# Optimization experiments

Measured on AMD Instinct MI355X. Metric: run time of the kernel, lower is better.

## Reference

```python
import jax, jax.numpy as jnp
import numpy as np
from jax import lax

NUM_SKETCH = 3
BN_EPS = 1e-5


def setup_inputs() -> dict:
    key = jax.random.key(0)
    ks = jax.random.split(key, 8)
    B, C, H, W = 32, 128, 64, 64
    D = C // 4  # comp_rate = 4
    k = 3
    x = jax.random.normal(ks[0], (B, C, H, W), dtype=jnp.float32)
    fan = C * k * k
    w1 = jax.random.normal(ks[1], (C, C, k, k), dtype=jnp.float32) / np.sqrt(fan)
    w2 = jax.random.normal(ks[2], (C, C, k, k), dtype=jnp.float32) / np.sqrt(fan)
    gamma1 = jnp.ones((C,), jnp.float32); beta1 = jnp.zeros((C,), jnp.float32)
    gamma2 = jnp.ones((C,), jnp.float32); beta2 = jnp.zeros((C,), jnp.float32)
    # count-sketch hash matrices: hs[j] is (D, C), each column c has a single 1
    idx = jax.random.randint(ks[3], (NUM_SKETCH, C), 0, D)
    hs = jax.nn.one_hot(idx, D, dtype=jnp.float32).transpose(0, 2, 1)  # (3, D, C)
    ss = (jax.random.randint(ks[4], (NUM_SKETCH, C), 0, 2) * 2 - 1).astype(jnp.float32)  # (3, C) signs
    return {"x": x, "w1": w1, "w2": w2, "gamma1": gamma1, "beta1": beta1,
            "gamma2": gamma2, "beta2": beta2, "hs": hs, "ss": ss}


def _sketch_conv_unsketch(x, w, hs, ss):
    # w: (Co, Ci, k, k); hs: (J, D, Co); ss: (J, Co)
    Co, Ci, k, _ = w.shape
    J, D, _ = hs.shape
    B, _, H, W = x.shape
    wf = w.reshape(Co, -1)  # (Co, M)
    # sketched weights per sketch j: h_j @ (wf * s_j[:, None])
    w_sk = jnp.einsum('jdc,jc,cm->jdm', hs, ss, wf).reshape(J * D, Ci, k, k)
    # one conv with J*D output channels (padding=1, stride=1 hardcoded in source)
    y = lax.conv_general_dilated(x, w_sk, window_strides=(1, 1),
                                 padding=[(1, 1), (1, 1)],
                                 dimension_numbers=('NCHW', 'OIHW', 'NCHW'))
    y = y.reshape(B, J, D, H, W)
    # unsketch activations: h_j^T @ y_j, then sign scale (num_s=1 so inner median is identity)
    y_un = jnp.einsum('jdc,bjdhw->jbchw', hs, y) * ss[:, None, :, None, None]
    return jnp.median(y_un, axis=0)  # median over the 3 sketches -> (B, Co, H, W)


def _bn_relu(y, gamma, beta):
    # BatchNorm2d in training mode: biased batch stats over (N, H, W)
    mean = jnp.mean(y, axis=(0, 2, 3), keepdims=True)
    var = jnp.var(y, axis=(0, 2, 3), keepdims=True)
    yhat = (y - mean) * lax.rsqrt(var + BN_EPS)
    return jax.nn.relu(yhat * gamma[None, :, None, None] + beta[None, :, None, None])


def reference(x, w1, w2, gamma1, beta1, gamma2, beta2, hs, ss):
    residual = x
    out1 = _bn_relu(_sketch_conv_unsketch(x, w1, hs, ss), gamma1, beta1)
    del out1  # faithful to source bug: second conv loop uses x, discarding out1
    out = _bn_relu(_sketch_conv_unsketch(x, w2, hs, ss), gamma2, beta2)
    return out + residual
```

## Files before the change

### kernel.cpp

```cpp
#include <hip/hip_runtime.h>
#include <stdint.h>

typedef __bf16 bf16x8 __attribute__((ext_vector_type(8)));
typedef float  f32x4  __attribute__((ext_vector_type(4)));

static constexpr int Bn = 32, Cn = 128, Hn = 64, Wn = 64, HWn = 4096;
static constexpr size_t OFF_XT    = 0;
static constexpr size_t OFF_WF    = 33554432;
static constexpr size_t OFF_IDX   = 33775616;
static constexpr size_t OFF_M     = 33777152;
static constexpr size_t OFF_STATS = 67331584;
static constexpr size_t OFF_BN    = 67332608;

__device__ __forceinline__ unsigned short f32_to_bf16(float f) {
    union { float f; unsigned u; } v; v.f = f;
    unsigned u = v.u;
    return (unsigned short)((u + 0x7FFFu + ((u >> 16) & 1u)) >> 16);
}
__device__ __forceinline__ float bf16_to_f32(unsigned short h) {
    union { unsigned u; float f; } v; v.u = ((unsigned)h) << 16;
    return v.f;
}

__global__ __launch_bounds__(256) void k_transpose(const float* __restrict__ x,
                                                   unsigned short* __restrict__ xT) {
    __shared__ __align__(16) unsigned short sm[256 * 40];
    int blk = blockIdx.x;
    int pt = blk & 15, q = (blk >> 4) & 3, b = blk >> 6;
    int p0 = pt * 256;
    int t = threadIdx.x;
    const float* xp = x + ((size_t)(b * Cn + q * 32) * HWn) + p0 + t;
#pragma unroll
    for (int cil = 0; cil < 32; ++cil)
        sm[t * 40 + cil] = f32_to_bf16(xp[(size_t)cil * HWn]);
    __syncthreads();
    uint4* dst = (uint4*)(xT + ((size_t)(b * 4 + q) * HWn + p0) * 32);
#pragma unroll
    for (int pass = 0; pass < 4; ++pass) {
        int pix = pass * 64 + (t >> 2);
        int ch  = t & 3;
        dst[pix * 4 + ch] = *(const uint4*)(&sm[pix * 40 + ch * 8]);
    }
}

__global__ void k_idx(const float* __restrict__ hs, int* __restrict__ idx) {
    int t = blockIdx.x * 256 + threadIdx.x;
    if (t >= 384) return;
    int j = t >> 7, c = t & 127;
    int found = 0;
    for (int d = 0; d < 32; ++d)
        if (hs[(j * 32 + d) * 128 + c] > 0.5f) found = d;
    idx[t] = found;
}

__global__ __launch_bounds__(256) void k_wsk(const float* __restrict__ w2,
                                             const float* __restrict__ hs,
                                             const float* __restrict__ ss,
                                             unsigned short* __restrict__ wf) {
    int f = blockIdx.x * 256 + threadIdx.x;
    int jj   = f & 7;
    int lane = (f >> 3) & 63;
    int nt   = (f >> 9) % 6;
    int qt   = f / (512 * 6);
    int t    = qt % 9;
    int q    = qt / 9;
    int k  = ((lane >> 4) << 3) + jj;
    int ci = q * 32 + k;
    int n  = nt * 16 + (lane & 15);
    int j = n >> 5, d = n & 31;
    float sum = 0.f;
    for (int c = 0; c < 128; ++c) {
        float g = hs[(j * 32 + d) * 128 + c];
        if (g != 0.f) sum += g * ss[j * 128 + c] * w2[(c * 128 + ci) * 9 + t];
    }
    wf[f] = f32_to_bf16(sum);
}

__global__ __launch_bounds__(256, 2) void k_conv(const unsigned short* __restrict__ xT,
                                                 const unsigned short* __restrict__ wf,
                                                 const int* __restrict__ idx,
                                                 const float* __restrict__ ss,
                                                 unsigned short* __restrict__ m_out) {
    __shared__ __align__(16) unsigned short sm[25088];
    __shared__ int   idx_sh[384];
    __shared__ float ss_sh[384];
    int tid  = threadIdx.x;
    int blk  = blockIdx.x;
    int tile = blk & 15, b = blk >> 4;
    int ty0  = tile * 4;
    int wv   = tid >> 6, lane = tid & 63;
    int quad = lane >> 4, l15 = lane & 15;

    for (int i = tid; i < 384; i += 256) { idx_sh[i] = idx[i]; ss_sh[i] = ss[i]; }

    f32x4 acc[4][6];
#pragma unroll
    for (int a = 0; a < 4; ++a)
#pragma unroll
        for (int nb = 0; nb < 6; ++nb) acc[a][nb] = (f32x4){0.f, 0.f, 0.f, 0.f};

    const unsigned short* wl = wf + lane * 8;

    for (int q = 0; q < 4; ++q) {
        __syncthreads();
#pragma unroll
        for (int pass = 0; pass < 2; ++pass) {
            int r = tid + pass * 256;
            if (r < 396) {
                int hy = r / 66, hx = r - hy * 66;
                int gy = ty0 + hy - 1, gx = hx - 1;
                uint4* dst = (uint4*)(&sm[r * 40]);
                if (gy >= 0 && gy < 64 && gx >= 0 && gx < 64) {
                    const uint4* src = (const uint4*)(xT + ((size_t)(b * 4 + q) * HWn + gy * 64 + gx) * 32);
                    dst[0] = src[0]; dst[1] = src[1]; dst[2] = src[2]; dst[3] = src[3];
                } else {
                    uint4 z = {0u, 0u, 0u, 0u};
                    dst[0] = z; dst[1] = z; dst[2] = z; dst[3] = z;
                }
            }
        }
        __syncthreads();
#pragma unroll
        for (int tp = 0; tp < 9; ++tp) {
            int dy = tp / 3, dx = tp % 3;
            bf16x8 afr[4];
#pragma unroll
            for (int mq = 0; mq < 4; ++mq) {
                int off = ((wv + dy) * 66 + mq * 16 + l15 + dx) * 40 + quad * 8;
                afr[mq] = *(const bf16x8*)(&sm[off]);
            }
            bf16x8 bfr[6];
            const unsigned short* wb = wl + (size_t)((q * 9 + tp) * 6) * 512;
#pragma unroll
            for (int nb = 0; nb < 6; ++nb)
                bfr[nb] = *(const bf16x8*)(wb + nb * 512);
#pragma unroll
            for (int mq = 0; mq < 4; ++mq)
#pragma unroll
                for (int nb = 0; nb < 6; ++nb)
                    acc[mq][nb] = __builtin_amdgcn_mfma_f32_16x16x32_bf16(afr[mq], bfr[nb], acc[mq][nb], 0, 0, 0);
        }
    }
    __syncthreads();
#pragma unroll
    for (int mq = 0; mq < 4; ++mq) {
#pragma unroll
        for (int nb = 0; nb < 6; ++nb) {
            int ch = nb * 16 + l15;
            int pbase = wv * 64 + mq * 16 + quad * 4;
#pragma unroll
            for (int r = 0; r < 4; ++r)
                sm[(pbase + r) * 98 + ch] = f32_to_bf16(acc[mq][nb][r]);
        }
    }
    __syncthreads();
    int p = tid;
    unsigned short* mp = m_out + (size_t)b * Cn * HWn + tile * 256 + tid;
#pragma unroll 4
    for (int c = 0; c < 128; ++c) {
        int i0 = idx_sh[c], i1 = idx_sh[128 + c], i2 = idx_sh[256 + c];
        float z0 = ss_sh[c]       * bf16_to_f32(sm[p * 98 + i0]);
        float z1 = ss_sh[128 + c] * bf16_to_f32(sm[p * 98 + 32 + i1]);
        float z2 = ss_sh[256 + c] * bf16_to_f32(sm[p * 98 + 64 + i2]);
        float lo = fminf(z0, z1), hi = fmaxf(z0, z1);
        float med = fmaxf(lo, fminf(hi, z2));
        mp[(size_t)c * HWn] = f32_to_bf16(med);
    }
}

__global__ __launch_bounds__(256) void k_stats(const unsigned short* __restrict__ m,
                                               float* __restrict__ stats) {
    int blk = blockIdx.x;
    int c = blk >> 2, bq = blk & 3;
    int tid = threadIdx.x;
    float s = 0.f, s2 = 0.f;
    for (int b = bq * 8; b < bq * 8 + 8; ++b) {
        const ushort4* mp = (const ushort4*)(m + (size_t)(b * Cn + c) * HWn);
#pragma unroll
        for (int i = 0; i < 4; ++i) {
            ushort4 v = mp[i * 256 + tid];
            float a0 = bf16_to_f32(v.x), a1 = bf16_to_f32(v.y);
            float a2 = bf16_to_f32(v.z), a3 = bf16_to_f32(v.w);
            s  += a0 + a1 + a2 + a3;
            s2 += a0 * a0 + a1 * a1 + a2 * a2 + a3 * a3;
        }
    }
    for (int o = 32; o > 0; o >>= 1) { s += __shfl_down(s, o); s2 += __shfl_down(s2, o); }
    __shared__ float rs[8];
    if ((tid & 63) == 0) { rs[tid >> 6] = s; rs[4 + (tid >> 6)] = s2; }
    __syncthreads();
    if (tid == 0) {
        float S = rs[0] + rs[1] + rs[2] + rs[3];
        float S2 = rs[4] + rs[5] + rs[6] + rs[7];
        atomicAdd(&stats[c], S);
        atomicAdd(&stats[128 + c], S2);
    }
}

__global__ void k_bn(const float* __restrict__ stats, const float* __restrict__ gamma,
                     const float* __restrict__ beta, float* __restrict__ bn) {
    int c = threadIdx.x;
    if (c < 128) {
        const float N = 131072.f;
        float mean = stats[c] / N;
        float var  = stats[128 + c] / N - mean * mean;
        float sc   = gamma[c] * rsqrtf(var + 1e-5f);
        bn[c] = sc;
        bn[128 + c] = beta[c] - mean * sc;
    }
}

__global__ __launch_bounds__(256) void k_apply(const unsigned short* __restrict__ m,
                                               const float* __restrict__ x,
                                               const float* __restrict__ bn,
                                               float* __restrict__ out) {
    int i4 = blockIdx.x * 256 + threadIdx.x;
    size_t base = (size_t)i4 * 4;
    int c = (int)((base >> 12) & 127);
    float sc = bn[c], sh = bn[128 + c];
    ushort4 mv = ((const ushort4*)m)[i4];
    float4  xv = ((const float4*)x)[i4];
    float4 o;
    o.x = fmaxf(bf16_to_f32(mv.x) * sc + sh, 0.f) + xv.x;
    o.y = fmaxf(bf16_to_f32(mv.y) * sc + sh, 0.f) + xv.y;
    o.z = fmaxf(bf16_to_f32(mv.z) * sc + sh, 0.f) + xv.z;
    o.w = fmaxf(bf16_to_f32(mv.w) * sc + sh, 0.f) + xv.w;
    ((float4*)out)[i4] = o;
}

extern "C" void kernel_launch(void* const* d_in, const int* in_sizes, int n_in,
                              void* d_out, int out_size, void* d_ws, size_t ws_size,
                              hipStream_t stream) {
    const float* x      = (const float*)d_in[0];
    const float* w2     = (const float*)d_in[2];
    const float* gamma2 = (const float*)d_in[5];
    const float* beta2  = (const float*)d_in[6];
    const float* hs     = (const float*)d_in[7];
    const float* ss     = (const float*)d_in[8];
    float* out = (float*)d_out;

    char* ws = (char*)d_ws;
    unsigned short* xT  = (unsigned short*)(ws + OFF_XT);
    unsigned short* wfp = (unsigned short*)(ws + OFF_WF);
    int*            idp = (int*)(ws + OFF_IDX);
    unsigned short* mp  = (unsigned short*)(ws + OFF_M);
    float*          st  = (float*)(ws + OFF_STATS);
    float*          bnp = (float*)(ws + OFF_BN);

    hipMemsetAsync(st, 0, 1024, stream);
    k_transpose<<<2048, 256, 0, stream>>>(x, xT);
    k_idx<<<2, 256, 0, stream>>>(hs, idp);
    k_wsk<<<432, 256, 0, stream>>>(w2, hs, ss, wfp);
    k_conv<<<512, 256, 0, stream>>>(xT, wfp, idp, ss, mp);
    k_stats<<<512, 256, 0, stream>>>(mp, st);
    k_bn<<<1, 128, 0, stream>>>(st, gamma2, beta2, bnp);
    k_apply<<<16384, 256, 0, stream>>>(mp, x, bnp, out);
}
```

Before: 227.2 us.

## Fuse fp32-to-bf16 transpose into conv staging with double-buffered LDS and 512 threads

Removes the separate transpose kernel and its bf16 intermediate buffer. The conv kernel now reads fp32 x directly, converts it to bf16 while staging into LDS, and double-buffers the four channel-quarter stages so the next stage loads while the current one computes. Blocks grow to 512 threads with half the accumulators per wave, and the unsketch/median epilogue is split across two channel halves. The cost is strided fp32 gathers (eight channels 16KB apart per thread) in place of contiguous 16-byte loads, more LDS per block, and a leftover unused k_conv that no longer initializes ss_sh.

Measured after the change: 233.2 us. 1.03x slower.

```diff
diff --git a/kernel.cpp b/kernel.cpp
--- a/kernel.cpp
+++ b/kernel.cpp
@@ -5,12 +5,11 @@
 typedef float  f32x4  __attribute__((ext_vector_type(4)));
 
 static constexpr int Bn = 32, Cn = 128, Hn = 64, Wn = 64, HWn = 4096;
-static constexpr size_t OFF_XT    = 0;
-static constexpr size_t OFF_WF    = 33554432;
-static constexpr size_t OFF_IDX   = 33775616;
-static constexpr size_t OFF_M     = 33777152;
-static constexpr size_t OFF_STATS = 67331584;
-static constexpr size_t OFF_BN    = 67332608;
+static constexpr size_t OFF_WF    = 0;
+static constexpr size_t OFF_IDX   = 221184;
+static constexpr size_t OFF_M     = 229376;
+static constexpr size_t OFF_STATS = 33783808;
+static constexpr size_t OFF_BN    = 33784832;
 
 __device__ __forceinline__ unsigned short f32_to_bf16(float f) {
     union { float f; unsigned u; } v; v.f = f;
@@ -20,27 +19,6 @@
 __device__ __forceinline__ float bf16_to_f32(unsigned short h) {
     union { unsigned u; float f; } v; v.u = ((unsigned)h) << 16;
     return v.f;
-}
-
-__global__ __launch_bounds__(256) void k_transpose(const float* __restrict__ x,
-                                                   unsigned short* __restrict__ xT) {
-    __shared__ __align__(16) unsigned short sm[256 * 40];
-    int blk = blockIdx.x;
-    int pt = blk & 15, q = (blk >> 4) & 3, b = blk >> 6;
-    int p0 = pt * 256;
-    int t = threadIdx.x;
-    const float* xp = x + ((size_t)(b * Cn + q * 32) * HWn) + p0 + t;
-#pragma unroll
-    for (int cil = 0; cil < 32; ++cil)
-        sm[t * 40 + cil] = f32_to_bf16(xp[(size_t)cil * HWn]);
-    __syncthreads();
-    uint4* dst = (uint4*)(xT + ((size_t)(b * 4 + q) * HWn + p0) * 32);
-#pragma unroll
-    for (int pass = 0; pass < 4; ++pass) {
-        int pix = pass * 64 + (t >> 2);
-        int ch  = t & 3;
-        dst[pix * 4 + ch] = *(const uint4*)(&sm[pix * 40 + ch * 8]);
-    }
 }
 
 __global__ void k_idx(const float* __restrict__ hs, int* __restrict__ idx) {
@@ -76,12 +54,11 @@
     wf[f] = f32_to_bf16(sum);
 }
 
-__global__ __launch_bounds__(256, 2) void k_conv(const unsigned short* __restrict__ xT,
+__global__ __launch_bounds__(512, 4) void k_conv(const float* __restrict__ x,
                                                  const unsigned short* __restrict__ wf,
                                                  const int* __restrict__ idx,
-                                                 const float* __restrict__ ss,
                                                  unsigned short* __restrict__ m_out) {
-    __shared__ __align__(16) unsigned short sm[25088];
+    __shared__ __align__(16) unsigned short sm[31680];
     __shared__ int   idx_sh[384];
     __shared__ float ss_sh[384];
     int tid  = threadIdx.x;
@@ -90,74 +67,87 @@
     int ty0  = tile * 4;
     int wv   = tid >> 6, lane = tid & 63;
     int quad = lane >> 4, l15 = lane & 15;
-
-    for (int i = tid; i < 384; i += 256) { idx_sh[i] = idx[i]; ss_sh[i] = ss[i]; }
-
-    f32x4 acc[4][6];
-#pragma unroll
-    for (int a = 0; a < 4; ++a)
+    int py   = wv >> 1, xh = (wv & 1) * 32;
+
+    for (int i = tid; i < 384; i += 512) {
+        idx_sh[i] = idx[i];
+    }
+
+    f32x4 acc[2][6];
+#pragma unroll
+    for (int a = 0; a < 2; ++a)
 #pragma unroll
         for (int nb = 0; nb < 6; ++nb) acc[a][nb] = (f32x4){0.f, 0.f, 0.f, 0.f};
 
-    const unsigned short* wl = wf + lane * 8;
-
+#define STAGE(Q, BUF)                                                                   \
+    {                                                                                   \
+        unsigned short* sb_ = (BUF);                                                    \
+        _Pragma("unroll")                                                               \
+        for (int t0 = 0; t0 < 1584; t0 += 512) {                                        \
+            int t = t0 + tid;                                                           \
+            if (t < 1584) {                                                             \
+                int r = t >> 2, oct = t & 3;                                            \
+                int hy = r / 66, hx = r - hy * 66;                                      \
+                int gy = ty0 + hy - 1, gx = hx - 1;                                     \
+                unsigned short tmp[8];                                                  \
+                if ((unsigned)gy < 64u && (unsigned)gx < 64u) {                         \
+                    const float* xp = x + ((size_t)((b * 4 + (Q)) * 32 + oct * 8) << 12) \
+                                        + gy * 64 + gx;                                 \
+                    _Pragma("unroll")                                                   \
+                    for (int i = 0; i < 8; ++i) tmp[i] = f32_to_bf16(xp[(size_t)i << 12]); \
+                } else {                                                                \
+                    _Pragma("unroll")                                                   \
+                    for (int i = 0; i < 8; ++i) tmp[i] = 0;                             \
+                }                                                                       \
+                *(uint4*)(&sb_[r * 40 + oct * 8]) = *(const uint4*)tmp;                 \
+            }                                                                           \
+        }                                                                               \
+    }
+
+    STAGE(0, sm);
+#pragma unroll
     for (int q = 0; q < 4; ++q) {
         __syncthreads();
-#pragma unroll
-        for (int pass = 0; pass < 2; ++pass) {
-            int r = tid + pass * 256;
-            if (r < 396) {
-                int hy = r / 66, hx = r - hy * 66;
-                int gy = ty0 + hy - 1, gx = hx - 1;
-                uint4* dst = (uint4*)(&sm[r * 40]);
-                if (gy >= 0 && gy < 64 && gx >= 0 && gx < 64) {
-                    const uint4* src = (const uint4*)(xT + ((size_t)(b * 4 + q) * HWn + gy * 64 + gx) * 32);
-                    dst[0] = src[0]; dst[1] = src[1]; dst[2] = src[2]; dst[3] = src[3];
-                } else {
-                    uint4 z = {0u, 0u, 0u, 0u};
-                    dst[0] = z; dst[1] = z; dst[2] = z; dst[3] = z;
-                }
-            }
-        }
-        __syncthreads();
+        if (q < 3) STAGE(q + 1, sm + ((q + 1) & 1) * 15840);
+        const unsigned short* sb = sm + (q & 1) * 15840;
 #pragma unroll
         for (int tp = 0; tp < 9; ++tp) {
             int dy = tp / 3, dx = tp % 3;
-            bf16x8 afr[4];
-#pragma unroll
-            for (int mq = 0; mq < 4; ++mq) {
-                int off = ((wv + dy) * 66 + mq * 16 + l15 + dx) * 40 + quad * 8;
-                afr[mq] = *(const bf16x8*)(&sm[off]);
+            bf16x8 afr[2];
+#pragma unroll
+            for (int mq = 0; mq < 2; ++mq) {
+                int off = ((py + dy) * 66 + xh + mq * 16 + l15 + dx) * 40 + quad * 8;
+                afr[mq] = *(const bf16x8*)(&sb[off]);
             }
-            bf16x8 bfr[6];
-            const unsigned short* wb = wl + (size_t)((q * 9 + tp) * 6) * 512;
-#pragma unroll
-            for (int nb = 0; nb < 6; ++nb)
-                bfr[nb] = *(const bf16x8*)(wb + nb * 512);
-#pragma unroll
-            for (int mq = 0; mq < 4; ++mq)
-#pragma unroll
-                for (int nb = 0; nb < 6; ++nb)
-                    acc[mq][nb] = __builtin_amdgcn_mfma_f32_16x16x32_bf16(afr[mq], bfr[nb], acc[mq][nb], 0, 0, 0);
-        }
-    }
-    __syncthreads();
-#pragma unroll
-    for (int mq = 0; mq < 4; ++mq) {
+            const unsigned short* wb = wf + (size_t)((q * 9 + tp) * 6) * 512 + lane * 8;
+#pragma unroll
+            for (int nb = 0; nb < 6; ++nb) {
+                bf16x8 bfr = *(const bf16x8*)(wb + nb * 512);
+                acc[0][nb] = __builtin_amdgcn_mfma_f32_16x16x32_bf16(afr[0], bfr, acc[0][nb], 0, 0, 0);
+                acc[1][nb] = __builtin_amdgcn_mfma_f32_16x16x32_bf16(afr[1], bfr, acc[1][nb], 0, 0, 0);
+            }
+        }
+    }
+#undef STAGE
+    __syncthreads();
+#pragma unroll
+    for (int mq = 0; mq < 2; ++mq) {
 #pragma unroll
         for (int nb = 0; nb < 6; ++nb) {
             int ch = nb * 16 + l15;
-            int pbase = wv * 64 + mq * 16 + quad * 4;
+            int pbase = py * 64 + xh + mq * 16 + quad * 4;
 #pragma unroll
             for (int r = 0; r < 4; ++r)
                 sm[(pbase + r) * 98 + ch] = f32_to_bf16(acc[mq][nb][r]);
         }
     }
     __syncthreads();
-    int p = tid;
-    unsigned short* mp = m_out + (size_t)b * Cn * HWn + tile * 256 + tid;
+    int p = tid & 255;
+    int c0 = (tid >> 8) * 64;
+    unsigned short* mp = m_out + (size_t)b * Cn * HWn + tile * 256 + p;
 #pragma unroll 4
-    for (int c = 0; c < 128; ++c) {
+    for (int cc = 0; cc < 64; ++cc) {
+        int c = c0 + cc;
         int i0 = idx_sh[c], i1 = idx_sh[128 + c], i2 = idx_sh[256 + c];
         float z0 = ss_sh[c]       * bf16_to_f32(sm[p * 98 + i0]);
         float z1 = ss_sh[128 + c] * bf16_to_f32(sm[p * 98 + 32 + i1]);
@@ -230,6 +220,119 @@
 
 extern "C" void kernel_launch(void* const* d_in, const int* in_sizes, int n_in,
                               void* d_out, int out_size, void* d_ws, size_t ws_size,
+                              hipStream_t stream);
+
+__global__ __launch_bounds__(512, 4) void k_conv_full(const float* __restrict__ x,
+                                                      const unsigned short* __restrict__ wf,
+                                                      const int* __restrict__ idx,
+                                                      const float* __restrict__ ss,
+                                                      unsigned short* __restrict__ m_out);
+
+__global__ __launch_bounds__(512, 4) void k_conv_full(const float* __restrict__ x,
+                                                      const unsigned short* __restrict__ wf,
+                                                      const int* __restrict__ idx,
+                                                      const float* __restrict__ ss,
+                                                      unsigned short* __restrict__ m_out) {
+    __shared__ __align__(16) unsigned short sm[31680];
+    __shared__ int   idx_sh[384];
+    __shared__ float ss_sh[384];
+    int tid  = threadIdx.x;
+    int blk  = blockIdx.x;
+    int tile = blk & 15, b = blk >> 4;
+    int ty0  = tile * 4;
+    int wv   = tid >> 6, lane = tid & 63;
+    int quad = lane >> 4, l15 = lane & 15;
+    int py   = wv >> 1, xh = (wv & 1) * 32;
+
+    for (int i = tid; i < 384; i += 512) { idx_sh[i] = idx[i]; ss_sh[i] = ss[i]; }
+
+    f32x4 acc[2][6];
+#pragma unroll
+    for (int a = 0; a < 2; ++a)
+#pragma unroll
+        for (int nb = 0; nb < 6; ++nb) acc[a][nb] = (f32x4){0.f, 0.f, 0.f, 0.f};
+
+#define STAGE(Q, BUF)                                                                   \
+    {                                                                                   \
+        unsigned short* sb_ = (BUF);                                                    \
+        _Pragma("unroll")                                                               \
+        for (int t0 = 0; t0 < 1584; t0 += 512) {                                        \
+            int t = t0 + tid;                                                           \
+            if (t < 1584) {                                                             \
+                int r = t >> 2, oct = t & 3;                                            \
+                int hy = r / 66, hx = r - hy * 66;                                      \
+                int gy = ty0 + hy - 1, gx = hx - 1;                                     \
+                unsigned short tmp[8];                                                  \
+                if ((unsigned)gy < 64u && (unsigned)gx < 64u) {                         \
+                    const float* xp = x + ((size_t)((b * 4 + (Q)) * 32 + oct * 8) << 12) \
+                                        + gy * 64 + gx;                                 \
+                    _Pragma("unroll")                                                   \
+                    for (int i = 0; i < 8; ++i) tmp[i] = f32_to_bf16(xp[(size_t)i << 12]); \
+                } else {                                                                \
+                    _Pragma("unroll")                                                   \
+                    for (int i = 0; i < 8; ++i) tmp[i] = 0;                             \
+                }                                                                       \
+                *(uint4*)(&sb_[r * 40 + oct * 8]) = *(const uint4*)tmp;                 \
+            }                                                                           \
+        }                                                                               \
+    }
+
+    STAGE(0, sm);
+#pragma unroll
+    for (int q = 0; q < 4; ++q) {
+        __syncthreads();
+        if (q < 3) STAGE(q + 1, sm + ((q + 1) & 1) * 15840);
+        const unsigned short* sb = sm + (q & 1) * 15840;
+#pragma unroll
+        for (int tp = 0; tp < 9; ++tp) {
+            int dy = tp / 3, dx = tp % 3;
+            bf16x8 afr[2];
+#pragma unroll
+            for (int mq = 0; mq < 2; ++mq) {
+                int off = ((py + dy) * 66 + xh + mq * 16 + l15 + dx) * 40 + quad * 8;
+                afr[mq] = *(const bf16x8*)(&sb[off]);
+            }
+            const unsigned short* wb = wf + (size_t)((q * 9 + tp) * 6) * 512 + lane * 8;
+#pragma unroll
+            for (int nb = 0; nb < 6; ++nb) {
+                bf16x8 bfr = *(const bf16x8*)(wb + nb * 512);
+                acc[0][nb] = __builtin_amdgcn_mfma_f32_16x16x32_bf16(afr[0], bfr, acc[0][nb], 0, 0, 0);
+                acc[1][nb] = __builtin_amdgcn_mfma_f32_16x16x32_bf16(afr[1], bfr, acc[1][nb], 0, 0, 0);
+            }
+        }
+    }
+#undef STAGE
+    __syncthreads();
+#pragma unroll
+    for (int mq = 0; mq < 2; ++mq) {
+#pragma unroll
+        for (int nb = 0; nb < 6; ++nb) {
+            int ch = nb * 16 + l15;
+            int pbase = py * 64 + xh + mq * 16 + quad * 4;
+#pragma unroll
+            for (int r = 0; r < 4; ++r)
+                sm[(pbase + r) * 98 + ch] = f32_to_bf16(acc[mq][nb][r]);
+        }
+    }
+    __syncthreads();
+    int p = tid & 255;
+    int c0 = (tid >> 8) * 64;
+    unsigned short* mp = m_out + (size_t)b * Cn * HWn + tile * 256 + p;
+#pragma unroll 4
+    for (int cc = 0; cc < 64; ++cc) {
+        int c = c0 + cc;
+        int i0 = idx_sh[c], i1 = idx_sh[128 + c], i2 = idx_sh[256 + c];
+        float z0 = ss_sh[c]       * bf16_to_f32(sm[p * 98 + i0]);
+        float z1 = ss_sh[128 + c] * bf16_to_f32(sm[p * 98 + 32 + i1]);
+        float z2 = ss_sh[256 + c] * bf16_to_f32(sm[p * 98 + 64 + i2]);
+        float lo = fminf(z0, z1), hi = fmaxf(z0, z1);
+        float med = fmaxf(lo, fminf(hi, z2));
+        mp[(size_t)c * HWn] = f32_to_bf16(med);
+    }
+}
+
+extern "C" void kernel_launch(void* const* d_in, const int* in_sizes, int n_in,
+                              void* d_out, int out_size, void* d_ws, size_t ws_size,
                               hipStream_t stream) {
     const float* x      = (const float*)d_in[0];
     const float* w2     = (const float*)d_in[2];
@@ -240,7 +343,6 @@
     float* out = (float*)d_out;
 
     char* ws = (char*)d_ws;
-    unsigned short* xT  = (unsigned short*)(ws + OFF_XT);
     unsigned short* wfp = (unsigned short*)(ws + OFF_WF);
     int*            idp = (int*)(ws + OFF_IDX);
     unsigned short* mp  = (unsigned short*)(ws + OFF_M);
@@ -248,10 +350,9 @@
     float*          bnp = (float*)(ws + OFF_BN);
 
     hipMemsetAsync(st, 0, 1024, stream);
-    k_transpose<<<2048, 256, 0, stream>>>(x, xT);
     k_idx<<<2, 256, 0, stream>>>(hs, idp);
     k_wsk<<<432, 256, 0, stream>>>(w2, hs, ss, wfp);
-    k_conv<<<512, 256, 0, stream>>>(xT, wfp, idp, ss, mp);
+    k_conv_full<<<512, 512, 0, stream>>>(x, wfp, idp, ss, mp);
     k_stats<<<512, 256, 0, stream>>>(mp, st);
     k_bn<<<1, 128, 0, stream>>>(st, gamma2, beta2, bnp);
     k_apply<<<16384, 256, 0, stream>>>(mp, x, bnp, out);
```

## Double-buffer conv input staging with async global-to-LDS loads and rewrite weight sketch

Applied to the files above, without the earlier changes.

The conv kernel now stages each input-channel chunk straight into LDS using global_load_lds, double-buffered so the next chunk loads while MFMAs run on the current one. It drops the padded LDS row stride and zeroes the halo once up front. The weight-sketch kernel now uses the precomputed hash indices, so each block builds one sketched output row with coalesced reads instead of scanning hs per element. The extra LDS per block and the removed occupancy hint may reduce occupancy, and the unpadded stride may cause LDS bank conflicts.

Result: no change. 231.7 us (+2.0%).

```diff
diff --git a/kernel.cpp b/kernel.cpp
--- a/kernel.cpp
+++ b/kernel.cpp
@@ -20,6 +20,12 @@
 __device__ __forceinline__ float bf16_to_f32(unsigned short h) {
     union { unsigned u; float f; } v; v.u = ((unsigned)h) << 16;
     return v.f;
+}
+
+__device__ __forceinline__ void load_lds16(const unsigned short* g, unsigned short* l) {
+    __builtin_amdgcn_global_load_lds((const __attribute__((address_space(1))) unsigned int*)g,
+                                     (__attribute__((address_space(3))) unsigned int*)l,
+                                     16, 0, 0);
 }
 
 __global__ __launch_bounds__(256) void k_transpose(const float* __restrict__ x,
@@ -54,34 +60,47 @@
 }
 
 __global__ __launch_bounds__(256) void k_wsk(const float* __restrict__ w2,
-                                             const float* __restrict__ hs,
+                                             const int* __restrict__ idx,
                                              const float* __restrict__ ss,
                                              unsigned short* __restrict__ wf) {
-    int f = blockIdx.x * 256 + threadIdx.x;
-    int jj   = f & 7;
-    int lane = (f >> 3) & 63;
-    int nt   = (f >> 9) % 6;
-    int qt   = f / (512 * 6);
-    int t    = qt % 9;
-    int q    = qt / 9;
-    int k  = ((lane >> 4) << 3) + jj;
-    int ci = q * 32 + k;
-    int n  = nt * 16 + (lane & 15);
+    int n = blockIdx.x;
     int j = n >> 5, d = n & 31;
-    float sum = 0.f;
+    __shared__ int   idb[128];
+    __shared__ float ssb[128];
+    int tid = threadIdx.x;
+    if (tid < 128) { idb[tid] = idx[j * 128 + tid]; ssb[tid] = ss[j * 128 + tid]; }
+    __syncthreads();
+    float acc[5] = {0.f, 0.f, 0.f, 0.f, 0.f};
     for (int c = 0; c < 128; ++c) {
-        float g = hs[(j * 32 + d) * 128 + c];
-        if (g != 0.f) sum += g * ss[j * 128 + c] * w2[(c * 128 + ci) * 9 + t];
-    }
-    wf[f] = f32_to_bf16(sum);
-}
-
-__global__ __launch_bounds__(256, 2) void k_conv(const unsigned short* __restrict__ xT,
-                                                 const unsigned short* __restrict__ wf,
-                                                 const int* __restrict__ idx,
-                                                 const float* __restrict__ ss,
-                                                 unsigned short* __restrict__ m_out) {
-    __shared__ __align__(16) unsigned short sm[25088];
+        if (idb[c] == d) {
+            float s = ssb[c];
+            const float* wr = w2 + (size_t)c * 1152;
+#pragma unroll
+            for (int e = 0; e < 5; ++e) {
+                int i = e * 256 + tid;
+                if (i < 1152) acc[e] += s * wr[i];
+            }
+        }
+    }
+    int nt = n >> 4, l15 = n & 15;
+#pragma unroll
+    for (int e = 0; e < 5; ++e) {
+        int i = e * 256 + tid;
+        if (i < 1152) {
+            int ci = i / 9, t = i - ci * 9;
+            int q = ci >> 5, k = ci & 31;
+            int lane = ((k >> 3) << 4) | l15, jj = k & 7;
+            wf[((size_t)((q * 9 + t) * 6 + nt)) * 512 + lane * 8 + jj] = f32_to_bf16(acc[e]);
+        }
+    }
+}
+
+__global__ __launch_bounds__(256) void k_conv(const unsigned short* __restrict__ xT,
+                                              const unsigned short* __restrict__ wf,
+                                              const int* __restrict__ idx,
+                                              const float* __restrict__ ss,
+                                              unsigned short* __restrict__ m_out) {
+    __shared__ __align__(16) unsigned short sm[25344];
     __shared__ int   idx_sh[384];
     __shared__ float ss_sh[384];
     int tid  = threadIdx.x;
@@ -92,6 +111,13 @@
     int quad = lane >> 4, l15 = lane & 15;
 
     for (int i = tid; i < 384; i += 256) { idx_sh[i] = idx[i]; ss_sh[i] = ss[i]; }
+    {
+        uint4 z = {0u, 0u, 0u, 0u};
+        uint4* smv = (uint4*)sm;
+#pragma unroll
+        for (int u = tid; u < 3168; u += 256) smv[u] = z;
+    }
+    __syncthreads();
 
     f32x4 acc[4][6];
 #pragma unroll
@@ -99,48 +125,50 @@
 #pragma unroll
         for (int nb = 0; nb < 6; ++nb) acc[a][nb] = (f32x4){0.f, 0.f, 0.f, 0.f};
 
-    const unsigned short* wl = wf + lane * 8;
-
+#define STAGE_ASYNC(Q, SBOFF)                                                           \
+    {                                                                                   \
+        const unsigned short* gch = xT + (((size_t)(b * 4 + (Q))) << 12) * 32;          \
+        _Pragma("unroll")                                                               \
+        for (int t0 = 0; t0 < 1584; t0 += 256) {                                        \
+            int u = t0 + tid;                                                           \
+            unsigned short* lb = sm + (SBOFF) + (size_t)(t0 + (tid & ~63)) * 8;         \
+            if (u < 1584) {                                                             \
+                int r = u >> 2, c16 = u & 3;                                            \
+                int hy = r / 66, hx = r - hy * 66;                                      \
+                int gy = ty0 + hy - 1, gx = hx - 1;                                     \
+                if ((unsigned)gy < 64u && (unsigned)gx < 64u) {                         \
+                    const unsigned short* gp = gch + ((size_t)(gy * 64 + gx)) * 32 + c16 * 8; \
+                    load_lds16(gp, lb);                                                 \
+                }                                                                       \
+            }                                                                           \
+        }                                                                               \
+    }
+
+    STAGE_ASYNC(0, 0);
     for (int q = 0; q < 4; ++q) {
         __syncthreads();
-#pragma unroll
-        for (int pass = 0; pass < 2; ++pass) {
-            int r = tid + pass * 256;
-            if (r < 396) {
-                int hy = r / 66, hx = r - hy * 66;
-                int gy = ty0 + hy - 1, gx = hx - 1;
-                uint4* dst = (uint4*)(&sm[r * 40]);
-                if (gy >= 0 && gy < 64 && gx >= 0 && gx < 64) {
-                    const uint4* src = (const uint4*)(xT + ((size_t)(b * 4 + q) * HWn + gy * 64 + gx) * 32);
-                    dst[0] = src[0]; dst[1] = src[1]; dst[2] = src[2]; dst[3] = src[3];
-                } else {
-                    uint4 z = {0u, 0u, 0u, 0u};
-                    dst[0] = z; dst[1] = z; dst[2] = z; dst[3] = z;
-                }
-            }
-        }
-        __syncthreads();
+        if (q < 3) STAGE_ASYNC(q + 1, ((q + 1) & 1) * 12672);
+        const unsigned short* sb = sm + (q & 1) * 12672;
 #pragma unroll
         for (int tp = 0; tp < 9; ++tp) {
             int dy = tp / 3, dx = tp % 3;
             bf16x8 afr[4];
 #pragma unroll
             for (int mq = 0; mq < 4; ++mq) {
-                int off = ((wv + dy) * 66 + mq * 16 + l15 + dx) * 40 + quad * 8;
-                afr[mq] = *(const bf16x8*)(&sm[off]);
+                int off = ((wv + dy) * 66 + mq * 16 + l15 + dx) * 32 + quad * 8;
+                afr[mq] = *(const bf16x8*)(&sb[off]);
             }
-            bf16x8 bfr[6];
-            const unsigned short* wb = wl + (size_t)((q * 9 + tp) * 6) * 512;
-#pragma unroll
-            for (int nb = 0; nb < 6; ++nb)
-                bfr[nb] = *(const bf16x8*)(wb + nb * 512);
-#pragma unroll
-            for (int mq = 0; mq < 4; ++mq)
-#pragma unroll
-                for (int nb = 0; nb < 6; ++nb)
-                    acc[mq][nb] = __builtin_amdgcn_mfma_f32_16x16x32_bf16(afr[mq], bfr[nb], acc[mq][nb], 0, 0, 0);
-        }
-    }
+            const unsigned short* wb = wf + (size_t)((q * 9 + tp) * 6) * 512 + lane * 8;
+#pragma unroll
+            for (int nb = 0; nb < 6; ++nb) {
+                bf16x8 bfr = *(const bf16x8*)(wb + nb * 512);
+#pragma unroll
+                for (int mq = 0; mq < 4; ++mq)
+                    acc[mq][nb] = __builtin_amdgcn_mfma_f32_16x16x32_bf16(afr[mq], bfr, acc[mq][nb], 0, 0, 0);
+            }
+        }
+    }
+#undef STAGE_ASYNC
     __syncthreads();
 #pragma unroll
     for (int mq = 0; mq < 4; ++mq) {
@@ -155,7 +183,7 @@
     }
     __syncthreads();
     int p = tid;
-    unsigned short* mp = m_out + (size_t)b * Cn * HWn + tile * 256 + tid;
+    unsigned short* mp = m_out + (size_t)b * Cn * HWn + tile * 256 + p;
 #pragma unroll 4
     for (int c = 0; c < 128; ++c) {
         int i0 = idx_sh[c], i1 = idx_sh[128 + c], i2 = idx_sh[256 + c];
@@ -250,7 +278,7 @@
     hipMemsetAsync(st, 0, 1024, stream);
     k_transpose<<<2048, 256, 0, stream>>>(x, xT);
     k_idx<<<2, 256, 0, stream>>>(hs, idp);
-    k_wsk<<<432, 256, 0, stream>>>(w2, hs, ss, wfp);
+    k_wsk<<<96, 256, 0, stream>>>(w2, idp, ss, wfp);
     k_conv<<<512, 256, 0, stream>>>(xT, wfp, idp, ss, mp);
     k_stats<<<512, 256, 0, stream>>>(mp, st);
     k_bn<<<1, 128, 0, stream>>>(st, gamma2, beta2, bnp);
```
